# Performance work log

Hardware: AMD Instinct MI355X
Metric: run time of the kernel (lower is better)

Reference implementation:

```python
import jax, jax.numpy as jnp
import numpy as np

L = 3        # number of GatedGCN layers
N = 30000    # nodes
E = 480000   # edges (avg degree 16)
D = 128      # hidden dim (= in_dim = out_dim)
IN = 128     # input feature dim
G = 64       # graphs in batch
C = 10       # classes


def setup_inputs() -> dict:
    key = jax.random.key(0)
    ks = jax.random.split(key, 32)
    s = 0.05  # weight scale to keep activations / sigmoid gates in a sane range
    inp = {
        "h": jax.random.normal(ks[0], (N, IN), jnp.float32),
        "e": jax.random.normal(ks[1], (E, IN), jnp.float32),
        "snorm_n": jax.random.uniform(ks[2], (N, 1), jnp.float32),
        "snorm_e": jax.random.uniform(ks[3], (E, 1), jnp.float32),
        "src": jax.random.randint(ks[4], (E,), 0, N, jnp.int32),
        "dst": jax.random.randint(ks[5], (E,), 0, N, jnp.int32),
        "graph_id": jnp.sort(jax.random.randint(ks[6], (N,), 0, G, jnp.int32)),
        # input embeddings
        "Wh_emb": jax.random.normal(ks[7], (IN, D), jnp.float32) * s,
        "bh_emb": jnp.zeros((D,), jnp.float32),
        "We_emb": jax.random.normal(ks[8], (IN, D), jnp.float32) * s,
        "be_emb": jnp.zeros((D,), jnp.float32),
        # per-layer A,B,C,D,E linears (stacked over L)
        "WA": jax.random.normal(ks[9], (L, D, D), jnp.float32) * s,
        "bA": jnp.zeros((L, D), jnp.float32),
        "WB": jax.random.normal(ks[10], (L, D, D), jnp.float32) * s,
        "bB": jnp.zeros((L, D), jnp.float32),
        "WC": jax.random.normal(ks[11], (L, D, D), jnp.float32) * s,
        "bC": jnp.zeros((L, D), jnp.float32),
        "WD": jax.random.normal(ks[12], (L, D, D), jnp.float32) * s,
        "bD": jnp.zeros((L, D), jnp.float32),
        "WE": jax.random.normal(ks[13], (L, D, D), jnp.float32) * s,
        "bE": jnp.zeros((L, D), jnp.float32),
        # batch-norm affine params (node / edge)
        "gn_h": jnp.ones((L, D), jnp.float32),
        "bt_h": jnp.zeros((L, D), jnp.float32),
        "gn_e": jnp.ones((L, D), jnp.float32),
        "bt_e": jnp.zeros((L, D), jnp.float32),
        # readout linear
        "Wr": jax.random.normal(ks[14], (D, C), jnp.float32) * s,
        "br": jnp.zeros((C,), jnp.float32),
    }
    return inp


def _bn(x, gamma, beta):
    # training-mode BatchNorm1d: biased batch stats over the node/edge axis
    mu = jnp.mean(x, axis=0)
    var = jnp.var(x, axis=0)
    return (x - mu) * jax.lax.rsqrt(var + 1e-5) * gamma + beta


def reference(h, e, snorm_n, snorm_e, src, dst, graph_id,
              Wh_emb, bh_emb, We_emb, be_emb,
              WA, bA, WB, bB, WC, bC, WD, bD, WE, bE,
              gn_h, bt_h, gn_e, bt_e, Wr, br):
    n_nodes = h.shape[0]
    h = h @ Wh_emb + bh_emb
    e = e @ We_emb + be_emb
    for l in range(WA.shape[0]):
        h_in, e_in = h, e
        Ah = h @ WA[l] + bA[l]
        Bh = h @ WB[l] + bB[l]
        Dh = h @ WD[l] + bD[l]
        Eh = h @ WE[l] + bE[l]
        Ce = e @ WC[l] + bC[l]
        # message: e_ij = Ce + Dh_src + Eh_dst ; gate = sigmoid(e_ij)
        e_new = Ce + Dh[src] + Eh[dst]                       # [E, D]
        sig = jax.nn.sigmoid(e_new)
        # reduce at dst: gated weighted mean of Bh_src
        num = jax.ops.segment_sum(sig * Bh[src], dst, num_segments=n_nodes)
        den = jax.ops.segment_sum(sig, dst, num_segments=n_nodes)
        h_new = Ah + num / (den + 1e-6)
        # graph norm
        h_new = h_new * snorm_n
        e_new = e_new * snorm_e
        # batch norm + ReLU + residual (dropout p=0 -> identity)
        h_new = jax.nn.relu(_bn(h_new, gn_h[l], bt_h[l]))
        e_new = jax.nn.relu(_bn(e_new, gn_e[l], bt_e[l]))
        h = h_in + h_new
        e = e_in + e_new
    # mean_nodes readout per graph, then linear classifier
    sums = jax.ops.segment_sum(h, graph_id, num_segments=G)
    cnt = jax.ops.segment_sum(jnp.ones((n_nodes, 1), h.dtype), graph_id, num_segments=G)
    hg = sums / jnp.maximum(cnt, 1.0)
    return hg @ Wr + br
```

## Files before the change

### kernel.cpp

```cpp
#include <hip/hip_runtime.h>
#include <cstdint>
#include <cstddef>

#define N_NODES  30000
#define N_EDGES  480000
#define N_LAYERS 3
#define N_GRAPHS 64
#define N_CLASS  10
#define NREP     32

typedef __attribute__((ext_vector_type(8))) short short8v;
typedef __attribute__((ext_vector_type(4))) float f32x4;

__device__ __forceinline__ unsigned short f2bf(float x) {
  union { float f; unsigned u; } v; v.f = x;
  unsigned r = v.u + 0x7FFFu + ((v.u >> 16) & 1u);
  return (unsigned short)(r >> 16);
}
__device__ __forceinline__ float bf2f(unsigned short h) {
  union { unsigned u; float f; } v; v.u = ((unsigned)h) << 16;
  return v.f;
}
__device__ __forceinline__ int swzW(int row, int off16) {
  return (row << 8) | (off16 ^ ((row & 7) << 4));
}

__global__ void wconv(const float* __restrict__ Wh, const float* __restrict__ We,
                      const float* __restrict__ WA, const float* __restrict__ WB,
                      const float* __restrict__ WC, const float* __restrict__ WD,
                      const float* __restrict__ WE, unsigned short* __restrict__ Wt)
{
  const int mi  = blockIdx.x >> 6;
  const int idx = (blockIdx.x & 63) * 256 + threadIdx.x;
  const float* src;
  if      (mi == 0) src = Wh;
  else if (mi == 1) src = We;
  else if (mi < 5)  src = WA + (size_t)(mi - 2) * 16384;
  else if (mi < 8)  src = WB + (size_t)(mi - 5) * 16384;
  else if (mi < 11) src = WC + (size_t)(mi - 8) * 16384;
  else if (mi < 14) src = WD + (size_t)(mi - 11) * 16384;
  else              src = WE + (size_t)(mi - 14) * 16384;
  const int k = idx >> 7, n = idx & 127;
  Wt[(size_t)mi * 16384 + (size_t)n * 128 + k] = f2bf(src[idx]);
}

struct GemmArgs {
  const unsigned short* Wt[4];
  const float* bias[4];
  unsigned short* out[4];
};

template<int NMAT, int AMODE>
__global__ __launch_bounds__(256)
void gemm_mm(const void* __restrict__ Ap, GemmArgs g, int M,
             const unsigned short* __restrict__ tb, const float2* __restrict__ pqh,
             unsigned short* __restrict__ hout,
             const unsigned short* __restrict__ WtX, const float* __restrict__ biasX)
{
  __shared__ __align__(16) unsigned char WL[32768];
  unsigned short* Wl = (unsigned short*)WL;
  const int t = threadIdx.x;
  const int w = t >> 6, l = t & 63;
  const int lr = l & 15, lkb = (l >> 4) * 8;
  const int r0 = blockIdx.x * 64;
  const bool vrow = (r0 + w * 16 + lr) < M;
  int arow = r0 + w * 16 + lr; if (arow >= M) arow = M - 1;

  short8v a[4];
  if (AMODE == 2) {
#pragma unroll
    for (int p = 0; p < 8; ++p) {
      const int ci = t + p * 256;
      *(short8v*)(WL + swzW(ci >> 4, (ci & 15) * 16)) = *(const short8v*)(WtX + (size_t)ci * 8);
    }
    const float* A = (const float*)Ap;
#pragma unroll
    for (int kk = 0; kk < 4; ++kk) {
      const float* p = A + (size_t)arow * 128 + kk * 32 + lkb;
      const float4 u = *(const float4*)p;
      const float4 v = *(const float4*)(p + 4);
      short8v av;
      av[0]=f2bf(u.x); av[1]=f2bf(u.y); av[2]=f2bf(u.z); av[3]=f2bf(u.w);
      av[4]=f2bf(v.x); av[5]=f2bf(v.y); av[6]=f2bf(v.z); av[7]=f2bf(v.w);
      a[kk] = av;
    }
    __syncthreads();
    f32x4 acc[8];
#pragma unroll
    for (int ct = 0; ct < 8; ++ct) acc[ct] = (f32x4){0.f, 0.f, 0.f, 0.f};
#pragma unroll
    for (int kk = 0; kk < 4; ++kk)
#pragma unroll
      for (int ct = 0; ct < 8; ++ct) {
        const short8v b = *(const short8v*)(WL + swzW(ct * 16 + lr, kk * 64 + (l >> 4) * 16));
        acc[ct] = __builtin_amdgcn_mfma_f32_16x16x32_bf16(a[kk], b, acc[ct], 0, 0, 0);
      }
    __syncthreads();
#pragma unroll
    for (int ct = 0; ct < 8; ++ct) {
      const float bb = biasX[ct * 16 + lr];
#pragma unroll
      for (int q = 0; q < 4; ++q)
        Wl[(w * 16 + (l >> 4) * 4 + q) * 136 + ct * 16 + lr] = f2bf(acc[ct][q] + bb);
    }
    __syncthreads();
#pragma unroll
    for (int kk = 0; kk < 4; ++kk) {
      a[kk] = *(const short8v*)(Wl + (w * 16 + lr) * 136 + kk * 32 + lkb);
      if (vrow) *(short8v*)(hout + (size_t)arow * 128 + kk * 32 + lkb) = a[kk];
    }
  } else if (AMODE == 1) {
    const unsigned short* A = (const unsigned short*)Ap;
#pragma unroll
    for (int kk = 0; kk < 4; ++kk) {
      const short8v tv = *(const short8v*)(tb + (size_t)arow * 128 + kk * 32 + lkb);
      const short8v hr = *(const short8v*)(A + (size_t)arow * 128 + kk * 32 + lkb);
      short8v av;
#pragma unroll
      for (int j = 0; j < 8; ++j) {
        const float2 PQ = pqh[kk * 32 + lkb + j];
        const float x = bf2f((unsigned short)tv[j]) * PQ.x + PQ.y;
        av[j] = (short)f2bf(bf2f((unsigned short)hr[j]) + fmaxf(x, 0.f));
      }
      a[kk] = av;
      if (vrow) *(short8v*)(hout + (size_t)arow * 128 + kk * 32 + lkb) = av;
    }
  } else {
    const unsigned short* A = (const unsigned short*)Ap;
#pragma unroll
    for (int kk = 0; kk < 4; ++kk)
      a[kk] = *(const short8v*)(A + (size_t)arow * 128 + kk * 32 + lkb);
  }

#pragma unroll
  for (int m = 0; m < NMAT; ++m) {
    if (m || AMODE == 2) __syncthreads();
#pragma unroll
    for (int p = 0; p < 8; ++p) {
      const int ci = t + p * 256;
      *(short8v*)(WL + swzW(ci >> 4, (ci & 15) * 16)) = *(const short8v*)(g.Wt[m] + (size_t)ci * 8);
    }
    __syncthreads();
    f32x4 acc[8];
#pragma unroll
    for (int ct = 0; ct < 8; ++ct) acc[ct] = (f32x4){0.f, 0.f, 0.f, 0.f};
#pragma unroll
    for (int kk = 0; kk < 4; ++kk)
#pragma unroll
      for (int ct = 0; ct < 8; ++ct) {
        const short8v b = *(const short8v*)(WL + swzW(ct * 16 + lr, kk * 64 + (l >> 4) * 16));
        acc[ct] = __builtin_amdgcn_mfma_f32_16x16x32_bf16(a[kk], b, acc[ct], 0, 0, 0);
      }
    __syncthreads();
#pragma unroll
    for (int ct = 0; ct < 8; ++ct) {
      const float bb = g.bias[m][ct * 16 + lr];
#pragma unroll
      for (int q = 0; q < 4; ++q)
        Wl[(w * 16 + (l >> 4) * 4 + q) * 136 + ct * 16 + lr] = f2bf(acc[ct][q] + bb);
    }
    __syncthreads();
    unsigned short* out = g.out[m];
#pragma unroll
    for (int p = 0; p < 4; ++p) {
      const int ci = t + p * 256;
      const int rr = ci >> 4, co = (ci & 15) * 8;
      const int grow = r0 + rr;
      if (grow < M)
        *(short8v*)(out + (size_t)grow * 128 + co) = *(const short8v*)(Wl + rr * 136 + co);
    }
  }
}

template<int LMODE>
__global__ __launch_bounds__(256)
void edge_kern(const float* __restrict__ e_in, const int* __restrict__ csr,
               unsigned short* __restrict__ eres, unsigned short* __restrict__ enew,
               const unsigned short* __restrict__ WtEmb, const float* __restrict__ bEmb,
               const unsigned short* __restrict__ WtC, const float* __restrict__ bC,
               const unsigned short* __restrict__ Dh, const unsigned short* __restrict__ Eh,
               const int* __restrict__ csrc, const int* __restrict__ cdst,
               const float* __restrict__ csne, const float2* __restrict__ pq)
{
  __shared__ __align__(16) unsigned char SM[32768];
  __shared__ __align__(16) unsigned short TB2[64 * 132];
  __shared__ float2 pql[128];
  const int t = threadIdx.x;
  const int w = t >> 6, l = t & 63;
  const int lr = l & 15, lkb = (l >> 4) * 8;
  const int r0 = blockIdx.x * 64;
  const int pos = r0 + w * 16 + lr;

  short8v a[4];
  f32x4 acc[8];

  if (LMODE == 0) {
#pragma unroll
    for (int p = 0; p < 8; ++p) {
      const int ci = t + p * 256;
      *(short8v*)(SM + swzW(ci >> 4, (ci & 15) * 16)) = *(const short8v*)(WtEmb + (size_t)ci * 8);
    }
#pragma unroll
    for (int p = 0; p < 4; ++p) {
      const int ci = t + p * 256;
      const int rr = ci >> 4, co = (ci & 15) * 8;
      const float* sp = e_in + (size_t)csr[r0 + rr] * 128 + co;
      const float4 u = *(const float4*)sp;
      const float4 v = *(const float4*)(sp + 4);
      short8v av;
      av[0]=f2bf(u.x); av[1]=f2bf(u.y); av[2]=f2bf(u.z); av[3]=f2bf(u.w);
      av[4]=f2bf(v.x); av[5]=f2bf(v.y); av[6]=f2bf(v.z); av[7]=f2bf(v.w);
      *(short8v*)(TB2 + rr * 132 + co) = av;
    }
    __syncthreads();
#pragma unroll
    for (int kk = 0; kk < 4; ++kk)
      a[kk] = *(const short8v*)(TB2 + (w * 16 + lr) * 132 + kk * 32 + lkb);
#pragma unroll
    for (int ct = 0; ct < 8; ++ct) acc[ct] = (f32x4){0.f, 0.f, 0.f, 0.f};
#pragma unroll
    for (int kk = 0; kk < 4; ++kk)
#pragma unroll
      for (int ct = 0; ct < 8; ++ct) {
        const short8v b = *(const short8v*)(SM + swzW(ct * 16 + lr, kk * 64 + (l >> 4) * 16));
        acc[ct] = __builtin_amdgcn_mfma_f32_16x16x32_bf16(a[kk], b, acc[ct], 0, 0, 0);
      }
    __syncthreads();
#pragma unroll
    for (int ct = 0; ct < 8; ++ct) {
      const float bb = bEmb[ct * 16 + lr];
#pragma unroll
      for (int q = 0; q < 4; ++q)
        TB2[(w * 16 + (l >> 4) * 4 + q) * 132 + ct * 16 + lr] = f2bf(acc[ct][q] + bb);
    }
#pragma unroll
    for (int p = 0; p < 8; ++p) {
      const int ci = t + p * 256;
      *(short8v*)(SM + swzW(ci >> 4, (ci & 15) * 16)) = *(const short8v*)(WtC + (size_t)ci * 8);
    }
    __syncthreads();
#pragma unroll
    for (int kk = 0; kk < 4; ++kk) {
      a[kk] = *(const short8v*)(TB2 + (w * 16 + lr) * 132 + kk * 32 + lkb);
      *(short8v*)(eres + (size_t)pos * 128 + kk * 32 + lkb) = a[kk];
    }
  } else {
    if (t < 128) pql[t] = pq[t];
#pragma unroll
    for (int p = 0; p < 8; ++p) {
      const int ci = t + p * 256;
      *(short8v*)(SM + swzW(ci >> 4, (ci & 15) * 16)) = *(const short8v*)(WtC + (size_t)ci * 8);
    }
    const float sn = csne[pos];
    short8v ep[4], er[4];
#pragma unroll
    for (int kk = 0; kk < 4; ++kk) {
      ep[kk] = *(const short8v*)(enew + (size_t)pos * 128 + kk * 32 + lkb);
      er[kk] = *(const short8v*)(eres + (size_t)pos * 128 + kk * 32 + lkb);
    }
    __syncthreads();
#pragma unroll
    for (int kk = 0; kk < 4; ++kk) {
      short8v av;
#pragma unroll
      for (int j = 0; j < 8; ++j) {
        const float2 PQ = pql[kk * 32 + lkb + j];
        const float x = bf2f((unsigned short)ep[kk][j]) * sn * PQ.x + PQ.y;
        av[j] = (short)f2bf(bf2f((unsigned short)er[kk][j]) + fmaxf(x, 0.f));
      }
      a[kk] = av;
      if (LMODE == 2)
        *(short8v*)(eres + (size_t)pos * 128 + kk * 32 + lkb) = av;
    }
  }

#pragma unroll
  for (int ct = 0; ct < 8; ++ct) acc[ct] = (f32x4){0.f, 0.f, 0.f, 0.f};
#pragma unroll
  for (int kk = 0; kk < 4; ++kk)
#pragma unroll
    for (int ct = 0; ct < 8; ++ct) {
      const short8v b = *(const short8v*)(SM + swzW(ct * 16 + lr, kk * 64 + (l >> 4) * 16));
      acc[ct] = __builtin_amdgcn_mfma_f32_16x16x32_bf16(a[kk], b, acc[ct], 0, 0, 0);
    }
  if (LMODE == 0) __syncthreads();
#pragma unroll
  for (int ct = 0; ct < 8; ++ct) {
    const float bb = bC[ct * 16 + lr];
#pragma unroll
    for (int q = 0; q < 4; ++q)
      TB2[(w * 16 + (l >> 4) * 4 + q) * 132 + ct * 16 + lr] = f2bf(acc[ct][q] + bb);
  }
  __syncthreads();
#pragma unroll
  for (int p = 0; p < 4; ++p) {
    const int ci = t + p * 256;
    const int rr = ci >> 4, co = (ci & 15) * 8;
    const int pp = r0 + rr;
    const int s = csrc[pp], d = cdst[pp];
    const short8v ce = *(const short8v*)(TB2 + rr * 132 + co);
    const short8v dv = *(const short8v*)(Dh + (size_t)s * 128 + co);
    const short8v ev = *(const short8v*)(Eh + (size_t)d * 128 + co);
    short8v ov;
#pragma unroll
    for (int j = 0; j < 8; ++j)
      ov[j] = (short)f2bf(bf2f((unsigned short)ce[j]) + bf2f((unsigned short)dv[j]) + bf2f((unsigned short)ev[j]));
    *(short8v*)(enew + (size_t)pp * 128 + co) = ov;
  }
}

__global__ void hist_kernel(const int* __restrict__ dst, int* __restrict__ cnt, int E)
{
  const int i = blockIdx.x * 256 + threadIdx.x;
  if (i < E) atomicAdd(&cnt[dst[i]], 1);
}

__global__ void scan_kernel(const int* __restrict__ cnt, int* __restrict__ start,
                            int* __restrict__ cursor, int n, int total)
{
  __shared__ int lds[1024];
  const int tid = threadIdx.x;
  const int chunk = (n + 1023) / 1024;
  const int lo = tid * chunk, hi = min(lo + chunk, n);
  int s = 0;
  for (int i = lo; i < hi; ++i) s += cnt[i];
  lds[tid] = s;
  __syncthreads();
  for (int off = 1; off < 1024; off <<= 1) {
    const int v = (tid >= off) ? lds[tid - off] : 0;
    __syncthreads();
    lds[tid] += v;
    __syncthreads();
  }
  int run = (tid == 0) ? 0 : lds[tid - 1];
  for (int i = lo; i < hi; ++i) { start[i] = run; cursor[i] = run; run += cnt[i]; }
  if (tid == 0) start[n] = total;
}

__global__ void scatter_kernel(const int* __restrict__ dst, const int* __restrict__ src,
                               const float* __restrict__ sne, int* __restrict__ cursor,
                               int* __restrict__ csr, int* __restrict__ csrc,
                               int* __restrict__ cdst, float* __restrict__ csne, int E)
{
  const int i = blockIdx.x * 256 + threadIdx.x;
  if (i < E) {
    const int p = atomicAdd(&cursor[dst[i]], 1);
    csr[p] = i; csrc[p] = src[i]; cdst[p] = dst[i]; csne[p] = sne[i];
  }
}

__global__ __launch_bounds__(256)
void aggregate(const unsigned short* __restrict__ enew, const unsigned short* __restrict__ Bh,
               const unsigned short* __restrict__ Ah, const float* __restrict__ snorm_n,
               const int* __restrict__ start, const int* __restrict__ csrc,
               const float* __restrict__ csne,
               unsigned short* __restrict__ tbuf, float* __restrict__ statrep, int doE)
{
  __shared__ float2 red[16][132];
  const int t = threadIdx.x;
  const int g = t >> 4, q = t & 15;
  const int v = blockIdx.x * 16 + g;
  const int s0 = start[v], s1 = start[v + 1];
  float num[8] = {0,0,0,0,0,0,0,0}, den[8] = {0,0,0,0,0,0,0,0};
  float psE[8] = {0,0,0,0,0,0,0,0}, pqE[8] = {0,0,0,0,0,0,0,0};

  float sn = 0.f;
  short8v ev = {}, bv = {};
  if (s0 < s1) {
    sn = csne[s0];
    ev = *(const short8v*)(enew + (size_t)s0 * 128 + q * 8);
    bv = *(const short8v*)(Bh + (size_t)csrc[s0] * 128 + q * 8);
  }
  for (int i = s0; i < s1; ++i) {
    float snn = 0.f;
    short8v evn = {}, bvn = {};
    if (i + 1 < s1) {
      snn = csne[i + 1];
      evn = *(const short8v*)(enew + (size_t)(i + 1) * 128 + q * 8);
      bvn = *(const short8v*)(Bh + (size_t)csrc[i + 1] * 128 + q * 8);
    }
#pragma unroll
    for (int j = 0; j < 8; ++j) {
      const float en = bf2f((unsigned short)ev[j]);
      const float sg = 1.f / (1.f + __expf(-en));
      num[j] = fmaf(sg, bf2f((unsigned short)bv[j]), num[j]);
      den[j] += sg;
      if (doE) { const float tv = en * sn; psE[j] += tv; pqE[j] = fmaf(tv, tv, pqE[j]); }
    }
    ev = evn; bv = bvn; sn = snn;
  }
  const float snv = snorm_n[v];
  const short8v av = *(const short8v*)(Ah + (size_t)v * 128 + q * 8);
  float hv[8];
  short8v tout;
#pragma unroll
  for (int j = 0; j < 8; ++j) {
    hv[j] = (bf2f((unsigned short)av[j]) + num[j] / (den[j] + 1e-6f)) * snv;
    tout[j] = (short)f2bf(hv[j]);
  }
  *(short8v*)(tbuf + (size_t)v * 128 + q * 8) = tout;

  float* rep = statrep + (size_t)(blockIdx.x & (NREP - 1)) * 512;
#pragma unroll
  for (int j = 0; j < 8; ++j) red[g][q * 8 + j] = make_float2(hv[j], hv[j] * hv[j]);
  __syncthreads();
  if (t < 128) {
    float s = 0.f, qq = 0.f;
    for (int gg = 0; gg < 16; ++gg) { s += red[gg][t].x; qq += red[gg][t].y; }
    atomicAdd(rep + t, s); atomicAdd(rep + 128 + t, qq);
  }
  if (doE) {
    __syncthreads();
#pragma unroll
    for (int j = 0; j < 8; ++j) red[g][q * 8 + j] = make_float2(psE[j], pqE[j]);
    __syncthreads();
    if (t < 128) {
      float s = 0.f, qq = 0.f;
      for (int gg = 0; gg < 16; ++gg) { s += red[gg][t].x; qq += red[gg][t].y; }
      atomicAdd(rep + 256 + t, s); atomicAdd(rep + 384 + t, qq);
    }
  }
}

__global__ void finalize_kernel(float* __restrict__ rep, float2* __restrict__ pqh,
                                float2* __restrict__ pqe,
                                const float* __restrict__ gn_h_l, const float* __restrict__ bt_h_l,
                                const float* __restrict__ gn_e_l, const float* __restrict__ bt_e_l,
                                float invN, float invE, int doE)
{
  const int c = threadIdx.x;
  float sH = 0.f, qH = 0.f, sE = 0.f, qE = 0.f;
  for (int r = 0; r < NREP; ++r) {
    float* p = rep + (size_t)r * 512;
    sH += p[c]; qH += p[128 + c]; sE += p[256 + c]; qE += p[384 + c];
    p[c] = 0.f; p[128 + c] = 0.f; p[256 + c] = 0.f; p[384 + c] = 0.f;
  }
  const float muH = sH * invN;
  const float vH  = fmaxf(qH * invN - muH * muH, 0.f);
  const float PH  = rsqrtf(vH + 1e-5f) * gn_h_l[c];
  pqh[c] = make_float2(PH, bt_h_l[c] - muH * PH);
  if (doE) {
    const float muE = sE * invE;
    const float vE  = fmaxf(qE * invE - muE * muE, 0.f);
    const float PE  = rsqrtf(vE + 1e-5f) * gn_e_l[c];
    pqe[c] = make_float2(PE, bt_e_l[c] - muE * PE);
  }
}

__global__ void readout_scatter(const unsigned short* __restrict__ h, const unsigned short* __restrict__ tb,
                                const float2* __restrict__ pqh, const int* __restrict__ gid,
                                float* __restrict__ gsum, int* __restrict__ gcnt, int N)
{
  const int c = threadIdx.x;
  const float2 PQ = pqh[c];
  const int row0 = blockIdx.x * 256;
  int cur = -1, cnt = 0;
  float s = 0.f;
  for (int r = 0; r < 256; ++r) {
    const int v = row0 + r;
    if (v >= N) break;
    const int g = gid[v];
    if (g != cur) {
      if (cur >= 0) {
        atomicAdd(&gsum[(size_t)cur * 128 + c], s);
        if (c == 0) atomicAdd(&gcnt[cur], cnt);
      }
      cur = g; s = 0.f; cnt = 0;
    }
    s += bf2f(h[(size_t)v * 128 + c]) + fmaxf(bf2f(tb[(size_t)v * 128 + c]) * PQ.x + PQ.y, 0.f);
    ++cnt;
  }
  if (cur >= 0) {
    atomicAdd(&gsum[(size_t)cur * 128 + c], s);
    if (c == 0) atomicAdd(&gcnt[cur], cnt);
  }
}

__global__ void readout_final(const float* __restrict__ gsum, const int* __restrict__ gcnt,
                              const float* __restrict__ Wr, const float* __restrict__ br,
                              float* __restrict__ out)
{
  const int g = blockIdx.x;
  const int t = threadIdx.x;
  __shared__ float hg[128];
  const float cnt = fmaxf((float)gcnt[g], 1.f);
  hg[t] = gsum[(size_t)g * 128 + t] / cnt;
  __syncthreads();
  if (t < N_CLASS) {
    float acc = br[t];
    for (int k = 0; k < 128; ++k) acc = fmaf(hg[k], Wr[k * N_CLASS + t], acc);
    out[g * N_CLASS + t] = acc;
  }
}

extern "C" void kernel_launch(void* const* d_in, const int* in_sizes, int n_in,
                              void* d_out, int out_size, void* d_ws, size_t ws_size,
                              hipStream_t stream)
{
  const float* h_in    = (const float*)d_in[0];
  const float* e_in    = (const float*)d_in[1];
  const float* snorm_n = (const float*)d_in[2];
  const float* snorm_e = (const float*)d_in[3];
  const int*   src     = (const int*)d_in[4];
  const int*   dst     = (const int*)d_in[5];
  const int*   gid     = (const int*)d_in[6];
  const float* Wh_emb  = (const float*)d_in[7];
  const float* bh_emb  = (const float*)d_in[8];
  const float* We_emb  = (const float*)d_in[9];
  const float* be_emb  = (const float*)d_in[10];
  const float* WA = (const float*)d_in[11]; const float* bA = (const float*)d_in[12];
  const float* WB = (const float*)d_in[13]; const float* bB = (const float*)d_in[14];
  const float* WC = (const float*)d_in[15]; const float* bC = (const float*)d_in[16];
  const float* WD = (const float*)d_in[17]; const float* bD = (const float*)d_in[18];
  const float* WE = (const float*)d_in[19]; const float* bE = (const float*)d_in[20];
  const float* gn_h = (const float*)d_in[21]; const float* bt_h = (const float*)d_in[22];
  const float* gn_e = (const float*)d_in[23]; const float* bt_e = (const float*)d_in[24];
  const float* Wr = (const float*)d_in[25]; const float* br = (const float*)d_in[26];
  float* out = (float*)d_out;
  (void)in_sizes; (void)n_in; (void)out_size; (void)ws_size;

  char* ws = (char*)d_ws;
  size_t off = 0;
  auto alloc = [&](size_t bytes) -> char* {
    off = (off + 255) & ~(size_t)255;
    char* p = ws + off;
    off += bytes;
    return p;
  };
  const size_t ND = (size_t)N_NODES * 128, ED = (size_t)N_EDGES * 128;
  unsigned short* hbuf = (unsigned short*)alloc(ND * 2);
  unsigned short* ebuf = (unsigned short*)alloc(ED * 2);
  unsigned short* enew = (unsigned short*)alloc(ED * 2);
  unsigned short* Ah   = (unsigned short*)alloc(ND * 2);
  unsigned short* Bh   = (unsigned short*)alloc(ND * 2);
  unsigned short* Dh   = (unsigned short*)alloc(ND * 2);
  unsigned short* Eh   = (unsigned short*)alloc(ND * 2);
  unsigned short* tbuf = (unsigned short*)alloc(ND * 2);
  unsigned short* Wt   = (unsigned short*)alloc((size_t)17 * 16384 * 2);
  float2* pqh          = (float2*)alloc(128 * 8);
  float2* pqe          = (float2*)alloc(128 * 8);
  int* start  = (int*)alloc((size_t)(N_NODES + 1) * 4);
  int* cursor = (int*)alloc((size_t)N_NODES * 4);
  int* csr    = (int*)alloc((size_t)N_EDGES * 4);
  int* csrc   = (int*)alloc((size_t)N_EDGES * 4);
  int* cdst   = (int*)alloc((size_t)N_EDGES * 4);
  float* csne = (float*)alloc((size_t)N_EDGES * 4);
  char* zbase = (char*)alloc(0);
  int*   cnt     = (int*)alloc((size_t)N_NODES * 4);
  float* statrep = (float*)alloc((size_t)NREP * 512 * 4);
  float* gsum    = (float*)alloc((size_t)N_GRAPHS * 128 * 4);
  int*   gcnt    = (int*)alloc((size_t)N_GRAPHS * 4);
  char* zend = (char*)alloc(0);

  hipMemsetAsync(zbase, 0, (size_t)(zend - zbase), stream);

  wconv<<<17 * 64, 256, 0, stream>>>(Wh_emb, We_emb, WA, WB, WC, WD, WE, Wt);

  hist_kernel<<<(N_EDGES + 255) / 256, 256, 0, stream>>>(dst, cnt, N_EDGES);
  scan_kernel<<<1, 1024, 0, stream>>>(cnt, start, cursor, N_NODES, N_EDGES);
  scatter_kernel<<<(N_EDGES + 255) / 256, 256, 0, stream>>>(dst, src, snorm_e, cursor,
                                                            csr, csrc, cdst, csne, N_EDGES);

  const int gbN = (N_NODES + 63) / 64;
  const int gbE = N_EDGES / 64;

  for (int l = 0; l < N_LAYERS; ++l) {
    const size_t bOff = (size_t)l * 128;
    const int doE = (l < N_LAYERS - 1) ? 1 : 0;
    {
      GemmArgs g{};
      g.Wt[0] = Wt + (size_t)(2 + l)  * 16384; g.bias[0] = bA + bOff; g.out[0] = Ah;
      g.Wt[1] = Wt + (size_t)(5 + l)  * 16384; g.bias[1] = bB + bOff; g.out[1] = Bh;
      g.Wt[2] = Wt + (size_t)(11 + l) * 16384; g.bias[2] = bD + bOff; g.out[2] = Dh;
      g.Wt[3] = Wt + (size_t)(14 + l) * 16384; g.bias[3] = bE + bOff; g.out[3] = Eh;
      if (l == 0)
        gemm_mm<4, 2><<<gbN, 256, 0, stream>>>(h_in, g, N_NODES, nullptr, nullptr, hbuf,
                                               Wt + 0 * 16384, bh_emb);
      else
        gemm_mm<4, 1><<<gbN, 256, 0, stream>>>(hbuf, g, N_NODES, tbuf, pqh, hbuf,
                                               nullptr, nullptr);
    }
    const unsigned short* WtC = Wt + (size_t)(8 + l) * 16384;
    if (l == 0)
      edge_kern<0><<<gbE, 256, 0, stream>>>(e_in, csr, ebuf, enew, Wt + 1 * 16384, be_emb,
                                            WtC, bC + bOff, Dh, Eh, csrc, cdst, csne, nullptr);
    else if (l == 1)
      edge_kern<2><<<gbE, 256, 0, stream>>>(nullptr, nullptr, ebuf, enew, nullptr, nullptr,
                                            WtC, bC + bOff, Dh, Eh, csrc, cdst, csne, pqe);
    else
      edge_kern<3><<<gbE, 256, 0, stream>>>(nullptr, nullptr, ebuf, enew, nullptr, nullptr,
                                            WtC, bC + bOff, Dh, Eh, csrc, cdst, csne, pqe);
    aggregate<<<N_NODES / 16, 256, 0, stream>>>(enew, Bh, Ah, snorm_n, start, csrc, csne,
                                                tbuf, statrep, doE);
    finalize_kernel<<<1, 128, 0, stream>>>(statrep, pqh, pqe, gn_h + bOff, bt_h + bOff,
                                           gn_e + bOff, bt_e + bOff,
                                           1.f / N_NODES, 1.f / N_EDGES, doE);
  }

  readout_scatter<<<(N_NODES + 255) / 256, 128, 0, stream>>>(hbuf, tbuf, pqh, gid, gsum, gcnt, N_NODES);
  readout_final<<<N_GRAPHS, 128, 0, stream>>>(gsum, gcnt, Wr, br, out);
}
```

Measured before the change: 919.9 us.

## Fuse gated aggregation and edge BN stats into edge kernel with boundary cleanup

The edge kernel now performs the gated sum aggregation per destination segment in dst-sorted order directly from LDS, writing finished node outputs when a segment lies fully inside the block and atomically accumulating partial num/den otherwise. A cleanup kernel finishes the boundary nodes and zeroes the partial buffers. Edge BN statistics are also computed in the fused kernel, and the last layer skips writing enew. This removes the separate aggregate pass that re-read enew from global memory. In exchange it adds a serial segmentation step on one thread, float atomics for split nodes, and more dynamic shared memory.

```diff
diff --git a/kernel.cpp b/kernel.cpp
--- a/kernel.cpp
+++ b/kernel.cpp
@@ -172,24 +172,43 @@
   }
 }
 
+#define MEGA_TAIL 2304
 template<int LMODE>
 __global__ __launch_bounds__(256)
-void edge_kern(const float* __restrict__ e_in, const int* __restrict__ csr,
+void edge_mega(const float* __restrict__ e_in, const int* __restrict__ csr,
                unsigned short* __restrict__ eres, unsigned short* __restrict__ enew,
                const unsigned short* __restrict__ WtEmb, const float* __restrict__ bEmb,
                const unsigned short* __restrict__ WtC, const float* __restrict__ bC,
                const unsigned short* __restrict__ Dh, const unsigned short* __restrict__ Eh,
+               const unsigned short* __restrict__ Bh, const unsigned short* __restrict__ Ah,
                const int* __restrict__ csrc, const int* __restrict__ cdst,
-               const float* __restrict__ csne, const float2* __restrict__ pq)
-{
-  __shared__ __align__(16) unsigned char SM[32768];
-  __shared__ __align__(16) unsigned short TB2[64 * 132];
-  __shared__ float2 pql[128];
+               const float* __restrict__ csne, const float* __restrict__ snorm_n,
+               const int* __restrict__ start, unsigned short* __restrict__ tbuf,
+               float* __restrict__ numb, float* __restrict__ denb,
+               float* __restrict__ statrep, const float2* __restrict__ pq)
+{
+  extern __shared__ __align__(16) char smem[];
+  char* SM = smem;
+  unsigned short* TB = (unsigned short*)((LMODE == 0) ? (smem + 32768) : smem);
+  char* tail = smem + ((LMODE == 0) ? 49664 : 32768);
+  float2* pql          = (float2*)tail;
+  int*    seg_node     = (int*)(tail + 1024);
+  int*    nb           = (int*)(tail + 1280);
+  int*    sb           = (int*)(tail + 1536);
+  float*  cne          = (float*)(tail + 1792);
+  unsigned short* seg_rowa = (unsigned short*)(tail + 2048);
+  int*    segKp        = (int*)(tail + 2180);
+  float2* red          = (float2*)SM;
+
   const int t = threadIdx.x;
   const int w = t >> 6, l = t & 63;
   const int lr = l & 15, lkb = (l >> 4) * 8;
   const int r0 = blockIdx.x * 64;
   const int pos = r0 + w * 16 + lr;
+  const int doE = (LMODE < 3);
+
+  if (t < 64) { nb[t] = cdst[r0 + t]; sb[t] = csrc[r0 + t]; cne[t] = csne[r0 + t]; }
+  if (LMODE >= 2 && t < 128) pql[t] = pq[t];
 
   short8v a[4];
   f32x4 acc[8];
@@ -210,12 +229,20 @@
       short8v av;
       av[0]=f2bf(u.x); av[1]=f2bf(u.y); av[2]=f2bf(u.z); av[3]=f2bf(u.w);
       av[4]=f2bf(v.x); av[5]=f2bf(v.y); av[6]=f2bf(v.z); av[7]=f2bf(v.w);
-      *(short8v*)(TB2 + rr * 132 + co) = av;
-    }
-    __syncthreads();
+      *(short8v*)(TB + rr * 132 + co) = av;
+    }
+    __syncthreads();
+    if (t == 0) {
+      int K = 0, prev = -1;
+      for (int j = 0; j < 64; ++j) {
+        const int v = nb[j];
+        if (v != prev) { seg_node[K] = v; seg_rowa[K] = (unsigned short)j; ++K; prev = v; }
+      }
+      seg_rowa[K] = 64; *segKp = K;
+    }
 #pragma unroll
     for (int kk = 0; kk < 4; ++kk)
-      a[kk] = *(const short8v*)(TB2 + (w * 16 + lr) * 132 + kk * 32 + lkb);
+      a[kk] = *(const short8v*)(TB + (w * 16 + lr) * 132 + kk * 32 + lkb);
 #pragma unroll
     for (int ct = 0; ct < 8; ++ct) acc[ct] = (f32x4){0.f, 0.f, 0.f, 0.f};
 #pragma unroll
@@ -231,7 +258,7 @@
       const float bb = bEmb[ct * 16 + lr];
 #pragma unroll
       for (int q = 0; q < 4; ++q)
-        TB2[(w * 16 + (l >> 4) * 4 + q) * 132 + ct * 16 + lr] = f2bf(acc[ct][q] + bb);
+        TB[(w * 16 + (l >> 4) * 4 + q) * 132 + ct * 16 + lr] = f2bf(acc[ct][q] + bb);
     }
 #pragma unroll
     for (int p = 0; p < 8; ++p) {
@@ -241,17 +268,15 @@
     __syncthreads();
 #pragma unroll
     for (int kk = 0; kk < 4; ++kk) {
-      a[kk] = *(const short8v*)(TB2 + (w * 16 + lr) * 132 + kk * 32 + lkb);
+      a[kk] = *(const short8v*)(TB + (w * 16 + lr) * 132 + kk * 32 + lkb);
       *(short8v*)(eres + (size_t)pos * 128 + kk * 32 + lkb) = a[kk];
     }
   } else {
-    if (t < 128) pql[t] = pq[t];
 #pragma unroll
     for (int p = 0; p < 8; ++p) {
       const int ci = t + p * 256;
       *(short8v*)(SM + swzW(ci >> 4, (ci & 15) * 16)) = *(const short8v*)(WtC + (size_t)ci * 8);
     }
-    const float sn = csne[pos];
     short8v ep[4], er[4];
 #pragma unroll
     for (int kk = 0; kk < 4; ++kk) {
@@ -259,6 +284,15 @@
       er[kk] = *(const short8v*)(eres + (size_t)pos * 128 + kk * 32 + lkb);
     }
     __syncthreads();
+    if (t == 0) {
+      int K = 0, prev = -1;
+      for (int j = 0; j < 64; ++j) {
+        const int v = nb[j];
+        if (v != prev) { seg_node[K] = v; seg_rowa[K] = (unsigned short)j; ++K; prev = v; }
+      }
+      seg_rowa[K] = 64; *segKp = K;
+    }
+    const float sn = cne[w * 16 + lr];
 #pragma unroll
     for (int kk = 0; kk < 4; ++kk) {
       short8v av;
@@ -283,29 +317,144 @@
       const short8v b = *(const short8v*)(SM + swzW(ct * 16 + lr, kk * 64 + (l >> 4) * 16));
       acc[ct] = __builtin_amdgcn_mfma_f32_16x16x32_bf16(a[kk], b, acc[ct], 0, 0, 0);
     }
-  if (LMODE == 0) __syncthreads();
+  __syncthreads();
 #pragma unroll
   for (int ct = 0; ct < 8; ++ct) {
     const float bb = bC[ct * 16 + lr];
 #pragma unroll
     for (int q = 0; q < 4; ++q)
-      TB2[(w * 16 + (l >> 4) * 4 + q) * 132 + ct * 16 + lr] = f2bf(acc[ct][q] + bb);
-  }
-  __syncthreads();
+      TB[(w * 16 + (l >> 4) * 4 + q) * 132 + ct * 16 + lr] = f2bf(acc[ct][q] + bb);
+  }
+  __syncthreads();
+  float psE[8] = {0,0,0,0,0,0,0,0}, pqE[8] = {0,0,0,0,0,0,0,0};
 #pragma unroll
   for (int p = 0; p < 4; ++p) {
     const int ci = t + p * 256;
     const int rr = ci >> 4, co = (ci & 15) * 8;
     const int pp = r0 + rr;
-    const int s = csrc[pp], d = cdst[pp];
-    const short8v ce = *(const short8v*)(TB2 + rr * 132 + co);
+    const int s = sb[rr], d = nb[rr];
+    const short8v ce = *(const short8v*)(TB + rr * 132 + co);
     const short8v dv = *(const short8v*)(Dh + (size_t)s * 128 + co);
     const short8v ev = *(const short8v*)(Eh + (size_t)d * 128 + co);
-    short8v ov;
+    short8v ob;
 #pragma unroll
     for (int j = 0; j < 8; ++j)
-      ov[j] = (short)f2bf(bf2f((unsigned short)ce[j]) + bf2f((unsigned short)dv[j]) + bf2f((unsigned short)ev[j]));
-    *(short8v*)(enew + (size_t)pp * 128 + co) = ov;
+      ob[j] = (short)f2bf(bf2f((unsigned short)ce[j]) + bf2f((unsigned short)dv[j]) + bf2f((unsigned short)ev[j]));
+    if (LMODE < 3) *(short8v*)(enew + (size_t)pp * 128 + co) = ob;
+    *(short8v*)(TB + rr * 132 + co) = ob;
+    if (doE) {
+      const float sn = cne[rr];
+#pragma unroll
+      for (int j = 0; j < 8; ++j) {
+        const float tv = bf2f((unsigned short)ob[j]) * sn;
+        psE[j] += tv; pqE[j] = fmaf(tv, tv, pqE[j]);
+      }
+    }
+  }
+  __syncthreads();
+  const int g = t >> 4, q = t & 15;
+  const int K = *segKp;
+  float hs[8] = {0,0,0,0,0,0,0,0}, hq[8] = {0,0,0,0,0,0,0,0};
+  for (int k = g; k < K; k += 16) {
+    const int ra = seg_rowa[k], rb = seg_rowa[k + 1];
+    const int v = seg_node[k];
+    const int s0 = start[v], s1 = start[v + 1];
+    float num[8] = {0,0,0,0,0,0,0,0}, den[8] = {0,0,0,0,0,0,0,0};
+    for (int r = ra; r < rb; ++r) {
+      const short8v e8 = *(const short8v*)(TB + r * 132 + q * 8);
+      const short8v b8 = *(const short8v*)(Bh + (size_t)sb[r] * 128 + q * 8);
+#pragma unroll
+      for (int j = 0; j < 8; ++j) {
+        const float en = bf2f((unsigned short)e8[j]);
+        const float sg = 1.f / (1.f + __expf(-en));
+        num[j] = fmaf(sg, bf2f((unsigned short)b8[j]), num[j]);
+        den[j] += sg;
+      }
+    }
+    if ((s1 - s0) == (rb - ra)) {
+      const float snv = snorm_n[v];
+      const short8v a8 = *(const short8v*)(Ah + (size_t)v * 128 + q * 8);
+      short8v to;
+#pragma unroll
+      for (int j = 0; j < 8; ++j) {
+        const float hv = (bf2f((unsigned short)a8[j]) + num[j] / (den[j] + 1e-6f)) * snv;
+        to[j] = (short)f2bf(hv);
+        hs[j] += hv; hq[j] = fmaf(hv, hv, hq[j]);
+      }
+      *(short8v*)(tbuf + (size_t)v * 128 + q * 8) = to;
+    } else {
+#pragma unroll
+      for (int j = 0; j < 8; ++j) {
+        atomicAdd(&numb[(size_t)v * 128 + q * 8 + j], num[j]);
+        atomicAdd(&denb[(size_t)v * 128 + q * 8 + j], den[j]);
+      }
+    }
+  }
+  __syncthreads();
+  float* rep = statrep + (size_t)(blockIdx.x & (NREP - 1)) * 512;
+#pragma unroll
+  for (int j = 0; j < 8; ++j) red[g * 132 + q * 8 + j] = make_float2(hs[j], hq[j]);
+  __syncthreads();
+  if (t < 128) {
+    float s = 0.f, qq = 0.f;
+    for (int gg = 0; gg < 16; ++gg) { s += red[gg * 132 + t].x; qq += red[gg * 132 + t].y; }
+    atomicAdd(rep + t, s); atomicAdd(rep + 128 + t, qq);
+  }
+  if (doE) {
+    __syncthreads();
+#pragma unroll
+    for (int j = 0; j < 8; ++j) red[g * 132 + q * 8 + j] = make_float2(psE[j], pqE[j]);
+    __syncthreads();
+    if (t < 128) {
+      float s = 0.f, qq = 0.f;
+      for (int gg = 0; gg < 16; ++gg) { s += red[gg * 132 + t].x; qq += red[gg * 132 + t].y; }
+      atomicAdd(rep + 256 + t, s); atomicAdd(rep + 384 + t, qq);
+    }
+  }
+}
+
+__global__ __launch_bounds__(256)
+void cleanup(float* __restrict__ numb, float* __restrict__ denb,
+             const unsigned short* __restrict__ Ah, const float* __restrict__ snorm_n,
+             const int* __restrict__ start, unsigned short* __restrict__ tbuf,
+             float* __restrict__ statrep)
+{
+  __shared__ float2 red[16][132];
+  const int t = threadIdx.x;
+  const int g = t >> 4, q = t & 15;
+  const int v = blockIdx.x * 16 + g;
+  const int s0 = start[v], s1 = start[v + 1];
+  const bool needs = (s0 == s1) || ((s0 >> 6) != ((s1 - 1) >> 6));
+  float hs[8] = {0,0,0,0,0,0,0,0}, hq[8] = {0,0,0,0,0,0,0,0};
+  if (needs) {
+    const float snv = snorm_n[v];
+    const short8v a8 = *(const short8v*)(Ah + (size_t)v * 128 + q * 8);
+    float* np = numb + (size_t)v * 128 + q * 8;
+    float* dp = denb + (size_t)v * 128 + q * 8;
+    const float4 n0 = *(const float4*)np, n1 = *(const float4*)(np + 4);
+    const float4 d0 = *(const float4*)dp, d1 = *(const float4*)(dp + 4);
+    const float num[8] = {n0.x,n0.y,n0.z,n0.w,n1.x,n1.y,n1.z,n1.w};
+    const float den[8] = {d0.x,d0.y,d0.z,d0.w,d1.x,d1.y,d1.z,d1.w};
+    short8v to;
+#pragma unroll
+    for (int j = 0; j < 8; ++j) {
+      const float hv = (bf2f((unsigned short)a8[j]) + num[j] / (den[j] + 1e-6f)) * snv;
+      to[j] = (short)f2bf(hv);
+      hs[j] = hv; hq[j] = hv * hv;
+    }
+    *(short8v*)(tbuf + (size_t)v * 128 + q * 8) = to;
+    const float4 z = make_float4(0.f, 0.f, 0.f, 0.f);
+    *(float4*)np = z; *(float4*)(np + 4) = z;
+    *(float4*)dp = z; *(float4*)(dp + 4) = z;
+  }
+#pragma unroll
+  for (int j = 0; j < 8; ++j) red[g][q * 8 + j] = make_float2(hs[j], hq[j]);
+  __syncthreads();
+  if (t < 128) {
+    float s = 0.f, qq = 0.f;
+    for (int gg = 0; gg < 16; ++gg) { s += red[gg][t].x; qq += red[gg][t].y; }
+    float* rep = statrep + (size_t)(blockIdx.x & (NREP - 1)) * 512;
+    atomicAdd(rep + t, s); atomicAdd(rep + 128 + t, qq);
   }
 }
 
@@ -346,79 +495,6 @@
   if (i < E) {
     const int p = atomicAdd(&cursor[dst[i]], 1);
     csr[p] = i; csrc[p] = src[i]; cdst[p] = dst[i]; csne[p] = sne[i];
-  }
-}
-
-__global__ __launch_bounds__(256)
-void aggregate(const unsigned short* __restrict__ enew, const unsigned short* __restrict__ Bh,
-               const unsigned short* __restrict__ Ah, const float* __restrict__ snorm_n,
-               const int* __restrict__ start, const int* __restrict__ csrc,
-               const float* __restrict__ csne,
-               unsigned short* __restrict__ tbuf, float* __restrict__ statrep, int doE)
-{
-  __shared__ float2 red[16][132];
-  const int t = threadIdx.x;
-  const int g = t >> 4, q = t & 15;
-  const int v = blockIdx.x * 16 + g;
-  const int s0 = start[v], s1 = start[v + 1];
-  float num[8] = {0,0,0,0,0,0,0,0}, den[8] = {0,0,0,0,0,0,0,0};
-  float psE[8] = {0,0,0,0,0,0,0,0}, pqE[8] = {0,0,0,0,0,0,0,0};
-
-  float sn = 0.f;
-  short8v ev = {}, bv = {};
-  if (s0 < s1) {
-    sn = csne[s0];
-    ev = *(const short8v*)(enew + (size_t)s0 * 128 + q * 8);
-    bv = *(const short8v*)(Bh + (size_t)csrc[s0] * 128 + q * 8);
-  }
-  for (int i = s0; i < s1; ++i) {
-    float snn = 0.f;
-    short8v evn = {}, bvn = {};
-    if (i + 1 < s1) {
-      snn = csne[i + 1];
-      evn = *(const short8v*)(enew + (size_t)(i + 1) * 128 + q * 8);
-      bvn = *(const short8v*)(Bh + (size_t)csrc[i + 1] * 128 + q * 8);
-    }
-#pragma unroll
-    for (int j = 0; j < 8; ++j) {
-      const float en = bf2f((unsigned short)ev[j]);
-      const float sg = 1.f / (1.f + __expf(-en));
-      num[j] = fmaf(sg, bf2f((unsigned short)bv[j]), num[j]);
-      den[j] += sg;
-      if (doE) { const float tv = en * sn; psE[j] += tv; pqE[j] = fmaf(tv, tv, pqE[j]); }
-    }
-    ev = evn; bv = bvn; sn = snn;
-  }
-  const float snv = snorm_n[v];
-  const short8v av = *(const short8v*)(Ah + (size_t)v * 128 + q * 8);
-  float hv[8];
-  short8v tout;
-#pragma unroll
-  for (int j = 0; j < 8; ++j) {
-    hv[j] = (bf2f((unsigned short)av[j]) + num[j] / (den[j] + 1e-6f)) * snv;
-    tout[j] = (short)f2bf(hv[j]);
-  }
-  *(short8v*)(tbuf + (size_t)v * 128 + q * 8) = tout;
-
-  float* rep = statrep + (size_t)(blockIdx.x & (NREP - 1)) * 512;
-#pragma unroll
-  for (int j = 0; j < 8; ++j) red[g][q * 8 + j] = make_float2(hv[j], hv[j] * hv[j]);
-  __syncthreads();
-  if (t < 128) {
-    float s = 0.f, qq = 0.f;
-    for (int gg = 0; gg < 16; ++gg) { s += red[gg][t].x; qq += red[gg][t].y; }
-    atomicAdd(rep + t, s); atomicAdd(rep + 128 + t, qq);
-  }
-  if (doE) {
-    __syncthreads();
-#pragma unroll
-    for (int j = 0; j < 8; ++j) red[g][q * 8 + j] = make_float2(psE[j], pqE[j]);
-    __syncthreads();
-    if (t < 128) {
-      float s = 0.f, qq = 0.f;
-      for (int gg = 0; gg < 16; ++gg) { s += red[gg][t].x; qq += red[gg][t].y; }
-      atomicAdd(rep + 256 + t, s); atomicAdd(rep + 384 + t, qq);
-    }
   }
 }
 
@@ -550,6 +626,8 @@
   float* statrep = (float*)alloc((size_t)NREP * 512 * 4);
   float* gsum    = (float*)alloc((size_t)N_GRAPHS * 128 * 4);
   int*   gcnt    = (int*)alloc((size_t)N_GRAPHS * 4);
+  float* numb    = (float*)alloc(ND * 4);
+  float* denb    = (float*)alloc(ND * 4);
   char* zend = (char*)alloc(0);
 
   hipMemsetAsync(zbase, 0, (size_t)(zend - zbase), stream);
@@ -563,6 +641,8 @@
 
   const int gbN = (N_NODES + 63) / 64;
   const int gbE = N_EDGES / 64;
+  const unsigned SH0 = 49664 + MEGA_TAIL;
+  const unsigned SH2 = 32768 + MEGA_TAIL;
 
   for (int l = 0; l < N_LAYERS; ++l) {
     const size_t bOff = (size_t)l * 128;
@@ -582,16 +662,18 @@
     }
     const unsigned short* WtC = Wt + (size_t)(8 + l) * 16384;
     if (l == 0)
-      edge_kern<0><<<gbE, 256, 0, stream>>>(e_in, csr, ebuf, enew, Wt + 1 * 16384, be_emb,
-                                            WtC, bC + bOff, Dh, Eh, csrc, cdst, csne, nullptr);
+      edge_mega<0><<<gbE, 256, SH0, stream>>>(e_in, csr, ebuf, enew, Wt + 1 * 16384, be_emb,
+                                              WtC, bC + bOff, Dh, Eh, Bh, Ah, csrc, cdst, csne,
+                                              snorm_n, start, tbuf, numb, denb, statrep, nullptr);
     else if (l == 1)
-      edge_kern<2><<<gbE, 256, 0, stream>>>(nullptr, nullptr, ebuf, enew, nullptr, nullptr,
-                                            WtC, bC + bOff, Dh, Eh, csrc, cdst, csne, pqe);
+      edge_mega<2><<<gbE, 256, SH2, stream>>>(nullptr, nullptr, ebuf, enew, nullptr, nullptr,
+                                              WtC, bC + bOff, Dh, Eh, Bh, Ah, csrc, cdst, csne,
+                                              snorm_n, start, tbuf, numb, denb, statrep, pqe);
     else
-      edge_kern<3><<<gbE, 256, 0, stream>>>(nullptr, nullptr, ebuf, enew, nullptr, nullptr,
-                                            WtC, bC + bOff, Dh, Eh, csrc, cdst, csne, pqe);
-    aggregate<<<N_NODES / 16, 256, 0, stream>>>(enew, Bh, Ah, snorm_n, start, csrc, csne,
-                                                tbuf, statrep, doE);
+      edge_mega<3><<<gbE, 256, SH2, stream>>>(nullptr, nullptr, ebuf, enew, nullptr, nullptr,
+                                              WtC, bC + bOff, Dh, Eh, Bh, Ah, csrc, cdst, csne,
+                                              snorm_n, start, tbuf, numb, denb, statrep, pqe);
+    cleanup<<<N_NODES / 16, 256, 0, stream>>>(numb, denb, Ah, snorm_n, start, tbuf, statrep);
     finalize_kernel<<<1, 128, 0, stream>>>(statrep, pqh, pqe, gn_h + bOff, bt_h + bOff,
                                            gn_e + bOff, bt_e + bOff,
                                            1.f / N_NODES, 1.f / N_EDGES, doE);
```

New measurement: 1.246 ms. 35.4% more time.
